# Kernel optimization log

Hardware: AMD Instinct MI355X
Metric: run time of the kernel (lower is better)

## Reference

```python
import jax, jax.numpy as jnp
import numpy as np

N_SEGMENT = 8
PATCH = 7          # correlation patch_size
RAD = PATCH // 2   # 3
EPS = 1e-5


def _bn(x, g, b):
    """BatchNorm (training-mode batch stats), channel axis = 1."""
    axes = tuple(i for i in range(x.ndim) if i != 1)
    m = x.mean(axes, keepdims=True)
    v = x.var(axes, keepdims=True)
    shp = [1] * x.ndim
    shp[1] = -1
    return (x - m) / jnp.sqrt(v + EPS) * g.reshape(shp) + b.reshape(shp)


def setup_inputs() -> dict:
    key = jax.random.key(0)
    ks = jax.random.split(key, 3)
    nt, c, h, w = 64, 64, 56, 56
    c_mid = c // 4                      # reduction=4 -> 16
    kk = PATCH * PATCH                  # corr_group=1 -> 49
    x = jax.random.normal(ks[0], (nt, c, h, w), dtype=jnp.float32)
    w21 = jax.random.normal(ks[1], (c_mid, c), dtype=jnp.float32) * (2.0 / c) ** 0.5
    w22 = jax.random.normal(ks[2], (c, kk), dtype=jnp.float32) * (2.0 / kk) ** 0.5
    return {
        "x": x, "w21": w21, "w22": w22,
        "g21": jnp.ones(c_mid), "b21": jnp.zeros(c_mid),
        "g22": jnp.ones(kk), "b22": jnp.zeros(kk),
        "g23": jnp.ones(c), "b23": jnp.zeros(c),
    }


def reference(x, w21, w22, g21, b21, g22, b22, g23, b23):
    nt, c, h, w = x.shape
    B = nt // N_SEGMENT
    residual = x

    # [B, c, T, h, w]
    xv = x.reshape(B, N_SEGMENT, c, h, w).transpose(0, 2, 1, 3, 4)
    # conv21: 1x1x1, c -> c_mid, no bias
    y = jnp.einsum('bcthw,oc->bothw', xv, w21)
    y = jax.nn.relu(_bn(y, g21, b21))          # [B, c_mid, T, h, w]

    # temporal shift: frame t pairs with frame t+1 (last with itself)
    idx = np.concatenate([np.arange(1, N_SEGMENT), [N_SEGMENT - 1]])
    y2 = y[:, :, idx]

    c_mid = y.shape[1]
    a = y.transpose(0, 2, 1, 3, 4).reshape(nt, c_mid, h, w)
    b2 = y2.transpose(0, 2, 1, 3, 4).reshape(nt, c_mid, h, w)

    # 7x7 local correlation (zero-padded), out[n, dy*7+dx, y, x] =
    #   sum_c a[n,c,y,x] * b2[n,c,y+dy-3,x+dx-3]
    bpad = jnp.pad(b2, ((0, 0), (0, 0), (RAD, RAD), (RAD, RAD)))
    corrs = [
        (a * bpad[:, :, dy:dy + h, dx:dx + w]).sum(axis=1)
        for dy in range(PATCH) for dx in range(PATCH)
    ]
    corr = jnp.stack(corrs, axis=1) / c_mid     # [nt, 49, h, w]

    corr = jax.nn.relu(_bn(corr, g22, b22))
    out = jnp.einsum('nkhw,ok->nohw', corr, w22)  # conv22: 1x1, 49 -> c
    out = _bn(out, g23, b23) + residual
    out = jax.nn.relu(out)
    return out  # net is identity
```

## Files before the change

### kernel.cpp

```cpp
#include <hip/hip_runtime.h>

#define HW 3136
#define W_ 56
#define C_IN 64
#define C_MID 16
#define KK 49
#define NT 64
#define NPIX (NT*HW)
#define NF 200704.0f
#define EPS 1e-5f

__global__ __launch_bounds__(256) void k1_conv(const float* __restrict__ x,
                                               const float* __restrict__ w21,
                                               float2* __restrict__ y2,
                                               float* __restrict__ st ) {
  float s[C_MID], q[C_MID];
#pragma unroll
  for (int o = 0; o < C_MID; ++o) { s[o] = 0.f; q[o] = 0.f; }

  for (int pix = blockIdx.x * 256 + threadIdx.x; pix < NPIX; pix += gridDim.x * 256) {
    int n = pix / HW; int hw = pix - n * HW;
    const float* xp = x + (size_t)n * C_IN * HW + hw;
    float acc[C_MID];
#pragma unroll
    for (int o = 0; o < C_MID; ++o) acc[o] = 0.f;
#pragma unroll
    for (int cb = 0; cb < C_IN; cb += 16) {
      float xv[16];
#pragma unroll
      for (int j = 0; j < 16; ++j) xv[j] = xp[(cb + j) * HW];
#pragma unroll
      for (int o = 0; o < C_MID; ++o) {
        float a = acc[o];
#pragma unroll
        for (int j = 0; j < 16; ++j) a = fmaf(w21[o * C_IN + cb + j], xv[j], a);
        acc[o] = a;
      }
    }
    float2* yp = y2 + (size_t)n * 8 * HW + hw;
#pragma unroll
    for (int c2 = 0; c2 < 8; ++c2) {
      yp[c2 * HW] = make_float2(acc[2 * c2], acc[2 * c2 + 1]);
    }
#pragma unroll
    for (int o = 0; o < C_MID; ++o) {
      s[o] += acc[o];
      q[o] += acc[o] * acc[o];
    }
  }

  __shared__ float combS[C_MID][4], combQ[C_MID][4];
  int wv = threadIdx.x >> 6;
  int lane = threadIdx.x & 63;
#pragma unroll
  for (int o = 0; o < C_MID; ++o) {
    float a = s[o], b = q[o];
#pragma unroll
    for (int off = 32; off > 0; off >>= 1) {
      a += __shfl_xor(a, off, 64);
      b += __shfl_xor(b, off, 64);
    }
    if (lane == 0) { combS[o][wv] = a; combQ[o][wv] = b; }
  }
  __syncthreads();
  if (threadIdx.x < 32) {
    int o = threadIdx.x & 15;
    float t = (threadIdx.x < 16)
      ? (combS[o][0] + combS[o][1] + combS[o][2] + combS[o][3])
      : (combQ[o][0] + combQ[o][1] + combQ[o][2] + combQ[o][3]);
    atomicAdd(&st[threadIdx.x], t);
  }
}

__global__ void k_fin(const float* __restrict__ s, const float* __restrict__ q,
                      const float* __restrict__ g, const float* __restrict__ b,
                      float* __restrict__ sc, float* __restrict__ sh, int C) {
  int i = threadIdx.x;
  if (i < C) {
    float m = s[i] * (1.0f / NF);
    float v = q[i] * (1.0f / NF) - m * m;
    float inv = g[i] / sqrtf(v + EPS);
    sc[i] = inv;
    sh[i] = fmaf(-m, inv, b[i]);
  }
}

#define TR 7
#define HR 13
#define HC 62
#define HSZ2 (HR*HC)
__global__ __launch_bounds__(392) void k3_corr(const float2* __restrict__ y2,
                                               const float* __restrict__ st ,
                                               const float* __restrict__ g21,
                                               const float* __restrict__ b21,
                                               float* __restrict__ corr) {
  __shared__ float2 Bl[8 * HSZ2];
  __shared__ float4 bn1[8];
  int tid = threadIdx.x;
  int n = blockIdx.x >> 3;
  int rt = blockIdx.x & 7;
  int r0 = rt * TR;
  int t = n & 7;
  int n2 = (n & ~7) | (t < 7 ? t + 1 : 7);

  if (tid < 8) {
    int cA = 2 * tid, cB = 2 * tid + 1;
    float mA = st[cA] * (1.0f / NF), mB = st[cB] * (1.0f / NF);
    float vA = st[16 + cA] * (1.0f / NF) - mA * mA;
    float vB = st[16 + cB] * (1.0f / NF) - mB * mB;
    float iA = g21[cA] / sqrtf(vA + EPS);
    float iB = g21[cB] / sqrtf(vB + EPS);
    bn1[tid] = make_float4(iA, fmaf(-mA, iA, b21[cA]), iB, fmaf(-mB, iB, b21[cB]));
  }
  __syncthreads();

  const float2* yb = y2 + (size_t)n2 * 8 * HW;
  for (int idx = tid; idx < 8 * HSZ2; idx += 392) {
    int c2 = idx / HSZ2; int rem = idx - c2 * HSZ2;
    int rr = rem / HC; int cc = rem - rr * HC;
    int gr = r0 + rr - 3; int gc = cc - 3;
    float2 v = make_float2(0.f, 0.f);
    if (gr >= 0 && gr < 56 && gc >= 0 && gc < 56) {
      float2 raw = yb[c2 * HW + gr * W_ + gc];
      float4 p = bn1[c2];
      v.x = fmaxf(fmaf(p.x, raw.x, p.y), 0.f);
      v.y = fmaxf(fmaf(p.z, raw.y, p.w), 0.f);
    }
    Bl[idx] = v;
  }

  int ty = tid / W_; int tx = tid - ty * W_;
  int r = r0 + ty;
  float2 a2[8];
  const float2* ya = y2 + (size_t)n * 8 * HW + r * W_ + tx;
#pragma unroll
  for (int c2 = 0; c2 < 8; ++c2) {
    float2 raw = ya[c2 * HW];
    float4 p = bn1[c2];
    a2[c2] = make_float2(fmaxf(fmaf(p.x, raw.x, p.y), 0.f),
                         fmaxf(fmaf(p.z, raw.y, p.w), 0.f));
  }

  __syncthreads();

  float* cp = corr + (size_t)n * KK * HW + r * W_ + tx;
#pragma unroll
  for (int dy = 0; dy < 7; ++dy) {
#pragma unroll
    for (int dx = 0; dx < 7; ++dx) {
      const float2* bp = Bl + (ty + dy) * HC + (tx + dx);
      float v0 = 0.f, v1 = 0.f;
#pragma unroll
      for (int c2 = 0; c2 < 8; ++c2) {
        float2 bv = bp[c2 * HSZ2];
        v0 = fmaf(a2[c2].x, bv.x, v0);
        v1 = fmaf(a2[c2].y, bv.y, v1);
      }
      cp[(dy * 7 + dx) * HW] = (v0 + v1) * (1.0f / 16.0f);
    }
  }
}

__global__ __launch_bounds__(256) void k3b_stats(const float* __restrict__ corr,
                                                 float* __restrict__ st ) {
  const float* base = corr + (size_t)blockIdx.x * HW;
  int k = blockIdx.x % KK;
  float s = 0.f, q = 0.f;
  const float4* b4 = (const float4*)base;
  for (int i = threadIdx.x; i < HW / 4; i += 256) {
    float4 v = b4[i];
    s += v.x + v.y + v.z + v.w;
    q += v.x * v.x + v.y * v.y + v.z * v.z + v.w * v.w;
  }
#pragma unroll
  for (int off = 32; off > 0; off >>= 1) {
    s += __shfl_xor(s, off, 64);
    q += __shfl_xor(q, off, 64);
  }
  __shared__ float rs[4], rq[4];
  int wv = threadIdx.x >> 6; int lane = threadIdx.x & 63;
  if (lane == 0) { rs[wv] = s; rq[wv] = q; }
  __syncthreads();
  if (threadIdx.x == 0) {
    atomicAdd(&st[k],      rs[0] + rs[1] + rs[2] + rs[3]);
    atomicAdd(&st[KK + k], rq[0] + rq[1] + rq[2] + rq[3]);
  }
}

__global__ __launch_bounds__(256, 3) void k5_mat(const float* __restrict__ corr,
                                                 const float* __restrict__ st ,
                                                 const float* __restrict__ g22,
                                                 const float* __restrict__ b22,
                                                 const float* __restrict__ w22,
                                                 float* __restrict__ tt) {
  __shared__ float bsc[KK], bsh[KK];
  if (threadIdx.x < KK) {
    int k = threadIdx.x;
    float m = st[k] * (1.0f / NF);
    float v = st[KK + k] * (1.0f / NF) - m * m;
    float inv = g22[k] / sqrtf(v + EPS);
    bsc[k] = inv;
    bsh[k] = fmaf(-m, inv, b22[k]);
  }
  __syncthreads();

  int pix = blockIdx.x * 256 + threadIdx.x;
  int n = pix / HW; int hw = pix - n * HW;
  const float* cp = corr + (size_t)n * KK * HW + hw;
  float cr[KK];
#pragma unroll
  for (int k = 0; k < KK; ++k)
    cr[k] = fmaxf(fmaf(bsc[k], cp[k * HW], bsh[k]), 0.f);

  float* tp = tt + (size_t)n * C_IN * HW + hw;
#pragma unroll 4
  for (int o = 0; o < 64; ++o) {
    const float* wr = w22 + o * KK;
    float t0 = 0.f, t1 = 0.f, t2 = 0.f, t3 = 0.f;
#pragma unroll
    for (int k = 0; k < 48; k += 4) {
      t0 = fmaf(wr[k],     cr[k],     t0);
      t1 = fmaf(wr[k + 1], cr[k + 1], t1);
      t2 = fmaf(wr[k + 2], cr[k + 2], t2);
      t3 = fmaf(wr[k + 3], cr[k + 3], t3);
    }
    t0 = fmaf(wr[48], cr[48], t0);
    tp[o * HW] = (t0 + t1) + (t2 + t3);
  }
}

__global__ __launch_bounds__(256) void k5b_stats(const float* __restrict__ tt,
                                                 float* __restrict__ st ) {
  const float4* b4 = (const float4*)(tt + (size_t)blockIdx.x * HW);
  int o = blockIdx.x & 63;
  float s = 0.f, q = 0.f;
  for (int i = threadIdx.x; i < HW / 4; i += 256) {
    float4 v = b4[i];
    s += v.x + v.y + v.z + v.w;
    q += v.x * v.x + v.y * v.y + v.z * v.z + v.w * v.w;
  }
#pragma unroll
  for (int off = 32; off > 0; off >>= 1) {
    s += __shfl_xor(s, off, 64);
    q += __shfl_xor(q, off, 64);
  }
  __shared__ float rs[4], rq[4];
  int wv = threadIdx.x >> 6; int lane = threadIdx.x & 63;
  if (lane == 0) { rs[wv] = s; rq[wv] = q; }
  __syncthreads();
  if (threadIdx.x == 0) {
    atomicAdd(&st[o],      rs[0] + rs[1] + rs[2] + rs[3]);
    atomicAdd(&st[64 + o], rq[0] + rq[1] + rq[2] + rq[3]);
  }
}

__global__ __launch_bounds__(256) void k7_ew(const float* __restrict__ tt,
                                             const float* __restrict__ st ,
                                             const float* __restrict__ g23,
                                             const float* __restrict__ b23,
                                             const float* __restrict__ x,
                                             float* __restrict__ out) {
  __shared__ float csc[64], csh[64];
  if (threadIdx.x < 64) {
    int o = threadIdx.x;
    float m = st[o] * (1.0f / NF);
    float v = st[64 + o] * (1.0f / NF) - m * m;
    float inv = g23[o] / sqrtf(v + EPS);
    csc[o] = inv;
    csh[o] = fmaf(-m, inv, b23[o]);
  }
  __syncthreads();

  const int tot4 = NPIX * C_IN / 4;
  const float4* t4 = (const float4*)tt;
  const float4* x4 = (const float4*)x;
  float4* o4 = (float4*)out;
  for (int i = blockIdx.x * 256 + threadIdx.x; i < tot4; i += gridDim.x * 256) {
    int plane = i / (HW / 4);
    int o = plane & 63;
    float a = csc[o], b = csh[o];
    float4 t = t4[i];
    float4 xv = x4[i];
    float4 r;
    r.x = fmaxf(fmaf(a, t.x, b) + xv.x, 0.f);
    r.y = fmaxf(fmaf(a, t.y, b) + xv.y, 0.f);
    r.z = fmaxf(fmaf(a, t.z, b) + xv.z, 0.f);
    r.w = fmaxf(fmaf(a, t.w, b) + xv.w, 0.f);
    o4[i] = r;
  }
}

__global__ __launch_bounds__(256, 3) void k5_stats(const float* __restrict__ corr,
                                                   const float* __restrict__ sc2,
                                                   const float* __restrict__ sh2,
                                                   const float* __restrict__ w22,
                                                   float* __restrict__ s3, float* __restrict__ q3) {
  __shared__ float aS[64], aQ[64];
  if (threadIdx.x < 64) { aS[threadIdx.x] = 0.f; aQ[threadIdx.x] = 0.f; }
  __syncthreads();
  int lane = threadIdx.x & 63;
  for (int pix = blockIdx.x * 256 + threadIdx.x; pix < NPIX; pix += gridDim.x * 256) {
    int n = pix / HW; int hw = pix - n * HW;
    const float* cp = corr + (size_t)n * KK * HW + hw;
    float cr[KK];
#pragma unroll
    for (int k = 0; k < KK; ++k)
      cr[k] = fmaxf(fmaf(sc2[k], cp[k * HW], sh2[k]), 0.f);
    for (int o = 0; o < 64; ++o) {
      const float* wr = w22 + o * KK;
      float t0 = 0.f, t1 = 0.f, t2 = 0.f, t3 = 0.f;
#pragma unroll
      for (int k = 0; k < 48; k += 4) {
        t0 = fmaf(wr[k],     cr[k],     t0);
        t1 = fmaf(wr[k + 1], cr[k + 1], t1);
        t2 = fmaf(wr[k + 2], cr[k + 2], t2);
        t3 = fmaf(wr[k + 3], cr[k + 3], t3);
      }
      t0 = fmaf(wr[48], cr[48], t0);
      float ttv = (t0 + t1) + (t2 + t3);
      float vs = ttv, vq = ttv * ttv;
#pragma unroll
      for (int off = 32; off > 0; off >>= 1) {
        vs += __shfl_xor(vs, off, 64);
        vq += __shfl_xor(vq, off, 64);
      }
      if (lane == 0) { atomicAdd(&aS[o], vs); atomicAdd(&aQ[o], vq); }
    }
  }
  __syncthreads();
  if (threadIdx.x < 64) {
    atomicAdd(&s3[threadIdx.x], aS[threadIdx.x]);
    atomicAdd(&q3[threadIdx.x], aQ[threadIdx.x]);
  }
}

__global__ __launch_bounds__(256, 3) void k7_out(const float* __restrict__ corr,
                                                 const float* __restrict__ sc2,
                                                 const float* __restrict__ sh2,
                                                 const float* __restrict__ w22,
                                                 const float* __restrict__ sc3,
                                                 const float* __restrict__ sh3,
                                                 const float* __restrict__ x,
                                                 float* __restrict__ out) {
  for (int pix = blockIdx.x * 256 + threadIdx.x; pix < NPIX; pix += gridDim.x * 256) {
    int n = pix / HW; int hw = pix - n * HW;
    const float* cp = corr + (size_t)n * KK * HW + hw;
    float cr[KK];
#pragma unroll
    for (int k = 0; k < KK; ++k)
      cr[k] = fmaxf(fmaf(sc2[k], cp[k * HW], sh2[k]), 0.f);
    const float* xp = x + (size_t)n * C_IN * HW + hw;
    float* op = out + (size_t)n * C_IN * HW + hw;
#pragma unroll 4
    for (int o = 0; o < 64; ++o) {
      const float* wr = w22 + o * KK;
      float t0 = 0.f, t1 = 0.f, t2 = 0.f, t3 = 0.f;
#pragma unroll
      for (int k = 0; k < 48; k += 4) {
        t0 = fmaf(wr[k],     cr[k],     t0);
        t1 = fmaf(wr[k + 1], cr[k + 1], t1);
        t2 = fmaf(wr[k + 2], cr[k + 2], t2);
        t3 = fmaf(wr[k + 3], cr[k + 3], t3);
      }
      t0 = fmaf(wr[48], cr[48], t0);
      float ttv = (t0 + t1) + (t2 + t3);
      float r = fmaf(sc3[o], ttv, sh3[o]) + xp[o * HW];
      op[o * HW] = fmaxf(r, 0.f);
    }
  }
}

extern "C" void kernel_launch(void* const* d_in, const int* in_sizes, int n_in,
                              void* d_out, int out_size, void* d_ws, size_t ws_size,
                              hipStream_t stream) {
  const float* x   = (const float*)d_in[0];
  const float* w21 = (const float*)d_in[1];
  const float* w22 = (const float*)d_in[2];
  const float* g21 = (const float*)d_in[3];
  const float* b21 = (const float*)d_in[4];
  const float* g22 = (const float*)d_in[5];
  const float* b22 = (const float*)d_in[6];
  const float* g23 = (const float*)d_in[7];
  const float* b23 = (const float*)d_in[8];
  float* out = (float*)d_out;

  const size_t Y_F    = (size_t)NT * C_MID * HW;
  const size_t CORR_F = (size_t)NT * KK * HW;
  const size_t TT_F   = (size_t)NT * C_IN * HW;
  const size_t ST_F   = 1024;

  float* ws   = (float*)d_ws;
  float2* y2  = (float2*)ws;
  float* corr = ws + Y_F;
  float* st   = corr + CORR_F;
  float* tt   = st + ST_F;

  float* s1 = st;          float* q1 = s1 + 16;
  float* s2 = q1 + 16;     float* q2 = s2 + KK;
  float* s3 = q2 + KK;     float* q3 = s3 + 64;
  float* sc2 = st + 300;   float* sh2 = sc2 + KK;
  float* sc3 = sh2 + KK;   float* sh3 = sc3 + 64;

  bool fast = ws_size >= (Y_F + CORR_F + ST_F + TT_F) * sizeof(float);

  hipMemsetAsync(st, 0, 258 * sizeof(float), stream);

  k1_conv  <<<784, 256, 0, stream>>>(x, w21, y2, s1);
  k3_corr  <<<512, 392, 0, stream>>>(y2, s1, g21, b21, corr);
  k3b_stats<<<NT * KK, 256, 0, stream>>>(corr, s2);

  if (fast) {
    k5_mat   <<<NPIX / 256, 256, 0, stream>>>(corr, s2, g22, b22, w22, tt);
    k5b_stats<<<NT * C_IN, 256, 0, stream>>>(tt, s3);
    k7_ew    <<<2048, 256, 0, stream>>>(tt, s3, g23, b23, x, out);
  } else {
    k_fin    <<<1, 64, 0, stream>>>(s2, q2, g22, b22, sc2, sh2, KK);
    k5_stats <<<512, 256, 0, stream>>>(corr, sc2, sh2, w22, s3, q3);
    k_fin    <<<1, 64, 0, stream>>>(s3, q3, g23, b23, sc3, sh3, C_IN);
    k7_out   <<<1024, 256, 0, stream>>>(corr, sc2, sh2, w22, sc3, sh3, x, out);
  }
}
```

Baseline: 294.1 us.

## Split conv21 into one-pixel-per-thread kernel and separate BN stats reduction kernel

The 1x1 conv kernel no longer loops over pixels or accumulates batch-norm sums. Each thread now loads all 64 input channels for one pixel and computes 16 outputs using four independent FMA chains. A new kernel re-reads the conv output to compute per-channel sum and sum-of-squares with float4 loads and one atomic per channel per block. This is meant to cut register pressure and improve occupancy in the conv, at the cost of an extra launch and an extra read of the intermediate tensor.

Result: no change. 293.5 us (-0.2%).

```diff
diff --git a/kernel.cpp b/kernel.cpp
--- a/kernel.cpp
+++ b/kernel.cpp
@@ -10,65 +10,64 @@
 #define NF 200704.0f
 #define EPS 1e-5f
 
-__global__ __launch_bounds__(256) void k1_conv(const float* __restrict__ x,
-                                               const float* __restrict__ w21,
-                                               float2* __restrict__ y2,
-                                               float* __restrict__ st ) {
-  float s[C_MID], q[C_MID];
-#pragma unroll
-  for (int o = 0; o < C_MID; ++o) { s[o] = 0.f; q[o] = 0.f; }
-
-  for (int pix = blockIdx.x * 256 + threadIdx.x; pix < NPIX; pix += gridDim.x * 256) {
-    int n = pix / HW; int hw = pix - n * HW;
-    const float* xp = x + (size_t)n * C_IN * HW + hw;
-    float acc[C_MID];
-#pragma unroll
-    for (int o = 0; o < C_MID; ++o) acc[o] = 0.f;
-#pragma unroll
-    for (int cb = 0; cb < C_IN; cb += 16) {
-      float xv[16];
-#pragma unroll
-      for (int j = 0; j < 16; ++j) xv[j] = xp[(cb + j) * HW];
-#pragma unroll
-      for (int o = 0; o < C_MID; ++o) {
-        float a = acc[o];
-#pragma unroll
-        for (int j = 0; j < 16; ++j) a = fmaf(w21[o * C_IN + cb + j], xv[j], a);
-        acc[o] = a;
-      }
-    }
-    float2* yp = y2 + (size_t)n * 8 * HW + hw;
-#pragma unroll
-    for (int c2 = 0; c2 < 8; ++c2) {
-      yp[c2 * HW] = make_float2(acc[2 * c2], acc[2 * c2 + 1]);
-    }
-#pragma unroll
-    for (int o = 0; o < C_MID; ++o) {
-      s[o] += acc[o];
-      q[o] += acc[o] * acc[o];
-    }
-  }
-
-  __shared__ float combS[C_MID][4], combQ[C_MID][4];
-  int wv = threadIdx.x >> 6;
-  int lane = threadIdx.x & 63;
+__global__ __launch_bounds__(256, 3) void k1_conv(const float* __restrict__ x,
+                                                  const float* __restrict__ w21,
+                                                  float2* __restrict__ y2) {
+  int pix = blockIdx.x * 256 + threadIdx.x;
+  int n = pix / HW; int hw = pix - n * HW;
+  const float* xp = x + (size_t)n * C_IN * HW + hw;
+
+  float xv[C_IN];
+#pragma unroll
+  for (int j = 0; j < C_IN; ++j) xv[j] = xp[j * HW];
+
+  float acc[C_MID];
+#pragma unroll
+  for (int o = 0; o < C_MID; ++o) acc[o] = 0.f;
 #pragma unroll
   for (int o = 0; o < C_MID; ++o) {
-    float a = s[o], b = q[o];
-#pragma unroll
-    for (int off = 32; off > 0; off >>= 1) {
-      a += __shfl_xor(a, off, 64);
-      b += __shfl_xor(b, off, 64);
-    }
-    if (lane == 0) { combS[o][wv] = a; combQ[o][wv] = b; }
-  }
-  __syncthreads();
-  if (threadIdx.x < 32) {
-    int o = threadIdx.x & 15;
-    float t = (threadIdx.x < 16)
-      ? (combS[o][0] + combS[o][1] + combS[o][2] + combS[o][3])
-      : (combQ[o][0] + combQ[o][1] + combQ[o][2] + combQ[o][3]);
-    atomicAdd(&st[threadIdx.x], t);
+    float a0 = 0.f, a1 = 0.f, a2 = 0.f, a3 = 0.f;
+    const float* wr = w21 + o * C_IN;
+#pragma unroll
+    for (int j = 0; j < C_IN; j += 4) {
+      a0 = fmaf(wr[j],     xv[j],     a0);
+      a1 = fmaf(wr[j + 1], xv[j + 1], a1);
+      a2 = fmaf(wr[j + 2], xv[j + 2], a2);
+      a3 = fmaf(wr[j + 3], xv[j + 3], a3);
+    }
+    acc[o] = (a0 + a1) + (a2 + a3);
+  }
+
+  float2* yp = y2 + (size_t)n * 8 * HW + hw;
+#pragma unroll
+  for (int c2 = 0; c2 < 8; ++c2)
+    yp[c2 * HW] = make_float2(acc[2 * c2], acc[2 * c2 + 1]);
+}
+
+__global__ __launch_bounds__(256) void k1b_stats(const float2* __restrict__ y2,
+                                                 float* __restrict__ st ) {
+  int c2 = blockIdx.x & 7;
+  const float4* b4 = (const float4*)(y2 + (size_t)blockIdx.x * HW);
+  float sA = 0.f, qA = 0.f, sB = 0.f, qB = 0.f;
+  for (int i = threadIdx.x; i < HW / 2; i += 256) {
+    float4 v = b4[i];
+    sA += v.x + v.z; qA += v.x * v.x + v.z * v.z;
+    sB += v.y + v.w; qB += v.y * v.y + v.w * v.w;
+  }
+#pragma unroll
+  for (int off = 32; off > 0; off >>= 1) {
+    sA += __shfl_xor(sA, off, 64); qA += __shfl_xor(qA, off, 64);
+    sB += __shfl_xor(sB, off, 64); qB += __shfl_xor(qB, off, 64);
+  }
+  __shared__ float r[4][4];
+  int wv = threadIdx.x >> 6; int lane = threadIdx.x & 63;
+  if (lane == 0) { r[wv][0] = sA; r[wv][1] = qA; r[wv][2] = sB; r[wv][3] = qB; }
+  __syncthreads();
+  if (threadIdx.x == 0) {
+    atomicAdd(&st[2 * c2],          r[0][0] + r[1][0] + r[2][0] + r[3][0]);
+    atomicAdd(&st[16 + 2 * c2],     r[0][1] + r[1][1] + r[2][1] + r[3][1]);
+    atomicAdd(&st[2 * c2 + 1],      r[0][2] + r[1][2] + r[2][2] + r[3][2]);
+    atomicAdd(&st[16 + 2 * c2 + 1], r[0][3] + r[1][3] + r[2][3] + r[3][3]);
   }
 }
 
@@ -405,7 +404,8 @@
 
   hipMemsetAsync(st, 0, 258 * sizeof(float), stream);
 
-  k1_conv  <<<784, 256, 0, stream>>>(x, w21, y2, s1);
+  k1_conv  <<<784, 256, 0, stream>>>(x, w21, y2);
+  k1b_stats<<<NT * 8, 256, 0, stream>>>(y2, s1);
   k3_corr  <<<512, 392, 0, stream>>>(y2, s1, g21, b21, corr);
   k3b_stats<<<NT * KK, 256, 0, stream>>>(corr, s2);
 
```
